# Kernel optimization log

Hardware: AMD Instinct MI355X
Metric: run time of the kernel (lower is better)

Reference implementation:

```python
import jax, jax.numpy as jnp
import numpy as np
from jax import lax

B, N, NIN, NOUT, K = 8, 4096, 64, 128, 32
RATIO, R = 0.25, 0.15
M = int(N * RATIO)
DIM = NIN + 4       # x_j concat 4 point-pair features


def setup_inputs() -> dict:
    key = jax.random.key(0)
    ks = jax.random.split(key, 10)
    x = jax.random.normal(ks[0], (B, N, NIN), jnp.float32)
    pos = jax.random.uniform(ks[1], (B, N, 3), jnp.float32)
    nrm = jax.random.normal(ks[2], (B, N, 3), jnp.float32)
    norm = nrm / jnp.linalg.norm(nrm, axis=-1, keepdims=True)
    batch = jnp.broadcast_to(jnp.arange(B, dtype=jnp.int32)[:, None], (B, N))
    s = 0.05
    W1 = jax.random.normal(ks[3], (DIM, DIM), jnp.float32) * s
    b1 = jnp.zeros((DIM,), jnp.float32)
    W2 = jax.random.normal(ks[4], (DIM, DIM), jnp.float32) * s
    b2 = jnp.zeros((DIM,), jnp.float32)
    W3 = jax.random.normal(ks[5], (DIM, NOUT), jnp.float32) * s
    b3 = jnp.zeros((NOUT,), jnp.float32)
    return dict(x=x, pos=pos, norm=norm, batch=batch,
                W1=W1, b1=b1, W2=W2, b2=b2, W3=W3, b3=b3)


def fps(pos):
    """Farthest point sampling, deterministic start at index 0. pos: [N,3] -> [M] int32."""
    n = pos.shape[0]
    def step(carry, _):
        dists, last = carry
        d = jnp.sum((pos - pos[last]) ** 2, axis=-1)
        dists = jnp.minimum(dists, d)
        nxt = jnp.argmax(dists).astype(jnp.int32)
        return (dists, nxt), last
    init = (jnp.full((n,), jnp.inf, pos.dtype), jnp.int32(0))
    (_, _), idx = lax.scan(step, init, None, length=M)
    return idx


def _angle(v1, v2):
    c = jnp.cross(v1, v2)
    return jnp.arctan2(jnp.linalg.norm(c, axis=-1), jnp.sum(v1 * v2, axis=-1))


def reference(x, pos, norm, batch, W1, b1, W2, b2, W3, b3):
    # batch is implicit in the leading B dim (equal-size clouds); arg kept for parity.
    idx = jax.vmap(fps)(pos)                                   # [B,M]
    pos_s = jnp.take_along_axis(pos, idx[..., None], axis=1)   # [B,M,3]
    norm_s = jnp.take_along_axis(norm, idx[..., None], axis=1) # [B,M,3]

    # radius neighbor search: K nearest within R per sampled center
    d2 = jnp.sum((pos_s[:, :, None, :] - pos[:, None, :, :]) ** 2, axis=-1)  # [B,M,N]
    masked = jnp.where(d2 <= R * R, d2, jnp.inf)
    negv, nbr = lax.top_k(-masked, K)                          # [B,M,K]
    valid = jnp.isfinite(negv)                                 # self always valid (d2=0)

    gather = jax.vmap(lambda a, i: a[i])                       # per-batch fancy gather
    x_j = gather(x, nbr)        # [B,M,K,NIN]
    pos_j = gather(pos, nbr)    # [B,M,K,3]
    norm_j = gather(norm, nbr)  # [B,M,K,3]

    d = pos_j - pos_s[:, :, None, :]                           # pos_j - pos_i
    n_i = jnp.broadcast_to(norm_s[:, :, None, :], norm_j.shape)
    ppf = jnp.stack([
        jnp.linalg.norm(d, axis=-1),
        _angle(n_i, d),
        _angle(norm_j, d),
        _angle(n_i, norm_j),
    ], axis=-1)                                                # [B,M,K,4]

    msg = jnp.concatenate([x_j, ppf], axis=-1)                 # [B,M,K,DIM]
    h = jax.nn.relu(msg @ W1 + b1)
    h = jax.nn.relu(h @ W2 + b2)
    h = jnp.where(valid[..., None], h, -jnp.inf)
    agg = jnp.max(h, axis=2)                                   # max aggregation [B,M,DIM]
    out = jax.nn.relu(agg @ W3 + b3)                           # global_nn [B,M,NOUT]
    return out, pos_s, idx
```

## Files before the change

### kernel.cpp

```cpp
#include <hip/hip_runtime.h>
#include <hip/hip_bf16.h>
#include <math.h>

#define BB 8
#define NN 4096
#define NIN 64
#define NOUTF 128
#define KNB 32
#define MM 1024
#define DIM 68
#define CAP 320

typedef float f32x2 __attribute__((ext_vector_type(2)));

template <int CTRL>
__device__ __forceinline__ float dppmax(float v)
{
    int m = __builtin_amdgcn_update_dpp(__float_as_int(v), __float_as_int(v),
                                        CTRL, 0xF, 0xF, false);
    return fmaxf(v, __int_as_float(m));
}

__global__ __launch_bounds__(256) void fps_kernel(
    const float* __restrict__ pos,
    int* __restrict__ idx_ws, float* __restrict__ pos_s_ws,
    float* __restrict__ out_pos_s, float* __restrict__ out_idx)
{
#pragma clang fp contract(off)
    __shared__ float4 redP[2][4];
    __shared__ int    redN[2][4];

    const int b    = blockIdx.x;
    const int tid  = threadIdx.x;
    const int wv   = tid >> 6;
    const int lane = tid & 63;
    const float* pb = pos + (size_t)b * NN * 3;

    f32x2 X[8], Y[8], Z[8], D[8];
#pragma unroll
    for (int j = 0; j < 8; ++j) {
        int pA = tid * 16 + 2 * j;
        X[j].x = pb[pA * 3 + 0]; X[j].y = pb[pA * 3 + 3];
        Y[j].x = pb[pA * 3 + 1]; Y[j].y = pb[pA * 3 + 4];
        Z[j].x = pb[pA * 3 + 2]; Z[j].y = pb[pA * 3 + 5];
        D[j].x = INFINITY;       D[j].y = INFINITY;
    }

    int   last = 0;
    float lx = pb[0], ly = pb[1], lz = pb[2];

    for (int t = 0; t < MM; ++t) {
        if (tid == 0) {
            idx_ws[b * MM + t]  = last;
            out_idx[b * MM + t] = (float)last;
            pos_s_ws[(b * MM + t) * 3 + 0] = lx;
            pos_s_ws[(b * MM + t) * 3 + 1] = ly;
            pos_s_ws[(b * MM + t) * 3 + 2] = lz;
            out_pos_s[(b * MM + t) * 3 + 0] = lx;
            out_pos_s[(b * MM + t) * 3 + 1] = ly;
            out_pos_s[(b * MM + t) * 3 + 2] = lz;
        }

        f32x2 lx2; lx2.x = lx; lx2.y = lx;
        f32x2 ly2; ly2.x = ly; ly2.y = ly;
        f32x2 lz2; lz2.x = lz; lz2.y = lz;

        float bv = -INFINITY;
        int   kloc = 0;
#pragma unroll
        for (int j = 0; j < 8; ++j) {
            f32x2 dx = X[j] - lx2;
            f32x2 dy = Y[j] - ly2;
            f32x2 dz = Z[j] - lz2;
            f32x2 s  = (dx * dx + dy * dy) + dz * dz;
            float n0 = fminf(D[j].x, s.x);
            float n1 = fminf(D[j].y, s.y);
            D[j].x = n0; D[j].y = n1;
            if (n0 > bv) { bv = n0; kloc = 2 * j; }
            if (n1 > bv) { bv = n1; kloc = 2 * j + 1; }
        }

        int jj = kloc >> 1;
        f32x2 xa = (jj & 1) ? X[1] : X[0];
        f32x2 xb = (jj & 1) ? X[3] : X[2];
        f32x2 xc = (jj & 1) ? X[5] : X[4];
        f32x2 xd = (jj & 1) ? X[7] : X[6];
        f32x2 xe = (jj & 2) ? xb : xa;
        f32x2 xf = (jj & 2) ? xd : xc;
        f32x2 xg = (jj & 4) ? xf : xe;
        float bx = (kloc & 1) ? xg.y : xg.x;

        f32x2 ya = (jj & 1) ? Y[1] : Y[0];
        f32x2 yb = (jj & 1) ? Y[3] : Y[2];
        f32x2 yc = (jj & 1) ? Y[5] : Y[4];
        f32x2 yd = (jj & 1) ? Y[7] : Y[6];
        f32x2 ye = (jj & 2) ? yb : ya;
        f32x2 yf = (jj & 2) ? yd : yc;
        f32x2 yg = (jj & 4) ? yf : ye;
        float by = (kloc & 1) ? yg.y : yg.x;

        f32x2 za = (jj & 1) ? Z[1] : Z[0];
        f32x2 zb = (jj & 1) ? Z[3] : Z[2];
        f32x2 zc = (jj & 1) ? Z[5] : Z[4];
        f32x2 zd = (jj & 1) ? Z[7] : Z[6];
        f32x2 ze = (jj & 2) ? zb : za;
        f32x2 zf = (jj & 2) ? zd : zc;
        f32x2 zg = (jj & 4) ? zf : ze;
        float bz = (kloc & 1) ? zg.y : zg.x;

        float r = bv;
        r = dppmax<0x111>(r);
        r = dppmax<0x112>(r);
        r = dppmax<0x114>(r);
        r = dppmax<0x118>(r);
        r = dppmax<0x142>(r);
        r = dppmax<0x143>(r);
        float wmax = __int_as_float(__builtin_amdgcn_readlane(__float_as_int(r), 63));

        unsigned long long msk = __ballot(bv == wmax);
        int wl = __ffsll(msk) - 1;

        const int p_ = t & 1;
        if (lane == wl) {
            redP[p_][wv] = make_float4(bx, by, bz, bv);
            redN[p_][wv] = tid * 16 + kloc;
        }
        __syncthreads();

        float4 e0 = redP[p_][0], e1 = redP[p_][1], e2 = redP[p_][2], e3 = redP[p_][3];
        int    i0 = redN[p_][0], i1 = redN[p_][1], i2 = redN[p_][2], i3 = redN[p_][3];

        float cv = e0.w; int ci = i0;
        float cx = e0.x, cy = e0.y, cz = e0.z;
        {
            bool bt = (e1.w > cv) || (e1.w == cv && i1 < ci);
            cv = bt ? e1.w : cv; ci = bt ? i1 : ci;
            cx = bt ? e1.x : cx; cy = bt ? e1.y : cy; cz = bt ? e1.z : cz;
        }
        {
            bool bt = (e2.w > cv) || (e2.w == cv && i2 < ci);
            cv = bt ? e2.w : cv; ci = bt ? i2 : ci;
            cx = bt ? e2.x : cx; cy = bt ? e2.y : cy; cz = bt ? e2.z : cz;
        }
        {
            bool bt = (e3.w > cv) || (e3.w == cv && i3 < ci);
            cv = bt ? e3.w : cv; ci = bt ? i3 : ci;
            cx = bt ? e3.x : cx; cy = bt ? e3.y : cy; cz = bt ? e3.z : cz;
        }
        last = ci; lx = cx; ly = cy; lz = cz;
    }
}

__global__ __launch_bounds__(256) void radius_kernel(
    const float* __restrict__ pos,
    const float* __restrict__ pos_s_ws,
    int* __restrict__ nbr_ws, int* __restrict__ nvalid_ws)
{
    __shared__ float d2L[4][CAP];
    __shared__ int   idL[4][CAP];
    __shared__ int   cntL[4];

    const int wv = threadIdx.x >> 6, lane = threadIdx.x & 63;
    const int c = blockIdx.x * 4 + wv;
    const int b = c >> 10;
    const float RSQ = 0.0225f;

    if (lane == 0) cntL[wv] = 0;

    float cx = pos_s_ws[c * 3 + 0];
    float cy = pos_s_ws[c * 3 + 1];
    float cz = pos_s_ws[c * 3 + 2];
    const float* pb = pos + (size_t)b * NN * 3;

    for (int it = 0; it < NN / 64; ++it) {
        int p = it * 64 + lane;
        float dx = __fsub_rn(cx, pb[p * 3 + 0]);
        float dy = __fsub_rn(cy, pb[p * 3 + 1]);
        float dz = __fsub_rn(cz, pb[p * 3 + 2]);
        float d2 = __fadd_rn(__fadd_rn(__fmul_rn(dx, dx), __fmul_rn(dy, dy)),
                             __fmul_rn(dz, dz));
        if (d2 <= RSQ) {
            int slot = atomicAdd(&cntL[wv], 1);
            if (slot < CAP) { d2L[wv][slot] = d2; idL[wv][slot] = p; }
        }
    }
    int n = cntL[wv];
    if (n > CAP) n = CAP;

    if (n <= KNB) {
        if (lane == 0) nvalid_ws[c] = n;
        if (lane < n) nbr_ws[c * KNB + lane] = idL[wv][lane];
    } else {
        if (lane == 0) nvalid_ws[c] = KNB;
        for (int a = lane; a < n; a += 64) {
            float da = d2L[wv][a]; int ia = idL[wv][a];
            int r = 0;
            for (int jj = 0; jj < n; ++jj) {
                float dj = d2L[wv][jj]; int ij = idL[wv][jj];
                r += (dj < da || (dj == da && ij < ia)) ? 1 : 0;
            }
            if (r < KNB) nbr_ws[c * KNB + r] = ia;
        }
    }
}

__device__ __forceinline__ float angle3(float ax, float ay, float az,
                                        float bx, float by, float bz)
{
    float cx = ay * bz - az * by;
    float cy = az * bx - ax * bz;
    float cz = ax * by - ay * bx;
    float cn = sqrtf(cx * cx + cy * cy + cz * cz);
    float dt = ax * bx + ay * by + az * bz;
    return atan2f(cn, dt);
}

__device__ __forceinline__ void layer_pass(const float* __restrict__ inL,
                                           const float* __restrict__ Ws,
                                           const float* __restrict__ bs,
                                           float* __restrict__ outL, int t)
{
    const int e = t & 63, wvi = t >> 6;
    for (int jg = wvi; jg < 17; jg += 4) {
        float ax = bs[jg * 4 + 0];
        float ay = bs[jg * 4 + 1];
        float az = bs[jg * 4 + 2];
        float aw = bs[jg * 4 + 3];
#pragma unroll 4
        for (int i = 0; i < DIM; ++i) {
            float m = inL[e * 69 + i];
            const float4 w = *reinterpret_cast<const float4*>(Ws + i * DIM + jg * 4);
            ax = fmaf(m, w.x, ax);
            ay = fmaf(m, w.y, ay);
            az = fmaf(m, w.z, az);
            aw = fmaf(m, w.w, aw);
        }
        outL[e * 69 + jg * 4 + 0] = fmaxf(ax, 0.0f);
        outL[e * 69 + jg * 4 + 1] = fmaxf(ay, 0.0f);
        outL[e * 69 + jg * 4 + 2] = fmaxf(az, 0.0f);
        outL[e * 69 + jg * 4 + 3] = fmaxf(aw, 0.0f);
    }
}

__global__ __launch_bounds__(256) void mlp_kernel(
    const float* __restrict__ x, const float* __restrict__ pos,
    const float* __restrict__ norm,
    const float* __restrict__ W1, const float* __restrict__ b1,
    const float* __restrict__ W2, const float* __restrict__ b2,
    const float* __restrict__ W3, const float* __restrict__ b3,
    const int* __restrict__ idx_ws, const float* __restrict__ pos_s_ws,
    const int* __restrict__ nbr_ws, const int* __restrict__ nvalid_ws,
    float* __restrict__ out)
{
    __shared__ alignas(16) float W1s[DIM * DIM];
    __shared__ alignas(16) float W2s[DIM * DIM];
    __shared__ float b1s[DIM], b2s[DIM];
    __shared__ float msgL[64 * 69];
    __shared__ float h1L[64 * 69];
    __shared__ float aggL[2 * DIM];
    __shared__ int   nvL[2], jLs[64];

    const int t = threadIdx.x;
    const int cg0 = blockIdx.x * 2;

    for (int u = t; u < DIM * DIM; u += 256) { W1s[u] = W1[u]; W2s[u] = W2[u]; }
    if (t < DIM) { b1s[t] = b1[t]; b2s[t] = b2[t]; }
    if (t < 2) nvL[t] = min(nvalid_ws[cg0 + t], KNB);
    __syncthreads();

    const int e = t & 63, fc = t >> 6;
    const int lc = e >> 5, slot = e & 31;
    const int c = cg0 + lc;
    const int b = c >> 10;

    if (fc == 0) {
        int nv = nvL[lc];
        jLs[e] = (slot < nv) ? nbr_ws[c * KNB + slot] : 0;
    }
    __syncthreads();

    const int j = jLs[e];
    {
        const float* xj = x + ((size_t)b * NN + j) * NIN + fc * 16;
#pragma unroll
        for (int r = 0; r < 4; ++r) {
            float4 v = *reinterpret_cast<const float4*>(xj + r * 4);
            msgL[e * 69 + fc * 16 + r * 4 + 0] = v.x;
            msgL[e * 69 + fc * 16 + r * 4 + 1] = v.y;
            msgL[e * 69 + fc * 16 + r * 4 + 2] = v.z;
            msgL[e * 69 + fc * 16 + r * 4 + 3] = v.w;
        }
    }
    if (fc == 0) {
        float pix = pos_s_ws[c * 3 + 0];
        float piy = pos_s_ws[c * 3 + 1];
        float piz = pos_s_ws[c * 3 + 2];
        int ic = idx_ws[c];
        const float* pj_ = pos  + ((size_t)b * NN + j) * 3;
        const float* nj_ = norm + ((size_t)b * NN + j) * 3;
        const float* ni_ = norm + ((size_t)b * NN + ic) * 3;
        float dx = pj_[0] - pix, dy = pj_[1] - piy, dz = pj_[2] - piz;
        float nix = ni_[0], niy = ni_[1], niz = ni_[2];
        float njx = nj_[0], njy = nj_[1], njz = nj_[2];
        msgL[e * 69 + 64] = sqrtf(dx * dx + dy * dy + dz * dz);
        msgL[e * 69 + 65] = angle3(nix, niy, niz, dx, dy, dz);
        msgL[e * 69 + 66] = angle3(njx, njy, njz, dx, dy, dz);
        msgL[e * 69 + 67] = angle3(nix, niy, niz, njx, njy, njz);
    }
    __syncthreads();

    layer_pass(msgL, W1s, b1s, h1L, t);
    __syncthreads();
    layer_pass(h1L, W2s, b2s, msgL, t);
    __syncthreads();

    if (t < 2 * DIM) {
        int cc = t / DIM, jf = t % DIM;
        int nv = nvL[cc];
        float v = -INFINITY;
        for (int s = 0; s < nv; ++s)
            v = fmaxf(v, msgL[(cc * 32 + s) * 69 + jf]);
        aggL[cc * DIM + jf] = v;
    }
    __syncthreads();

    {
        int cc = t >> 7, o = t & 127;
        int cgl = cg0 + cc;
        float acc = b3[o];
#pragma unroll 4
        for (int i = 0; i < DIM; ++i)
            acc = fmaf(aggL[cc * DIM + i], W3[i * NOUTF + o], acc);
        out[(size_t)cgl * NOUTF + o] = fmaxf(acc, 0.0f);
    }
}

extern "C" void kernel_launch(void* const* d_in, const int* in_sizes, int n_in,
                              void* d_out, int out_size, void* d_ws, size_t ws_size,
                              hipStream_t stream)
{
    const float* x    = (const float*)d_in[0];
    const float* pos  = (const float*)d_in[1];
    const float* norm = (const float*)d_in[2];
    const float* W1 = (const float*)d_in[4];
    const float* b1 = (const float*)d_in[5];
    const float* W2 = (const float*)d_in[6];
    const float* b2 = (const float*)d_in[7];
    const float* W3 = (const float*)d_in[8];
    const float* b3 = (const float*)d_in[9];

    float* out       = (float*)d_out;
    float* out_pos_s = out + (size_t)BB * MM * NOUTF;
    float* out_idx   = out_pos_s + (size_t)BB * MM * 3;

    char* ws = (char*)d_ws;
    int*   idx_ws    = (int*)ws;
    float* pos_s_ws  = (float*)(ws + 32768);
    int*   nbr_ws    = (int*)(ws + 131072);
    int*   nvalid_ws = (int*)(ws + 131072 + (size_t)BB * MM * KNB * 4);

    fps_kernel<<<dim3(BB), dim3(256), 0, stream>>>(pos, idx_ws, pos_s_ws,
                                                   out_pos_s, out_idx);
    radius_kernel<<<dim3((BB * MM) / 4), dim3(256), 0, stream>>>(pos, pos_s_ws,
                                                                 nbr_ws, nvalid_ws);
    mlp_kernel<<<dim3((BB * MM) / 2), dim3(256), 0, stream>>>(
        x, pos, norm, W1, b1, W2, b2, W3, b3,
        idx_ws, pos_s_ws, nbr_ws, nvalid_ws, out);
}
```

Before: 1.196 ms.

## Widen FPS block to 512 threads and defer argmax index recovery to winner lane

The FPS kernel now runs 512 threads with 8 points per thread instead of 256 with 16, halving the serial per-thread distance update per iteration. The per-thread argmax becomes a packed max tree, and the winning point's index and coordinates are recovered only in the winning lane by equality search after the wave reduction. The cross-wave reduction grows from 4 to 8 entries, and equality-based index recovery picks the lowest local index, which keeps tie behaviour consistent with first-occurrence argmax.

```diff
diff --git a/kernel.cpp b/kernel.cpp
--- a/kernel.cpp
+++ b/kernel.cpp
@@ -13,6 +13,15 @@
 
 typedef float f32x2 __attribute__((ext_vector_type(2)));
 
+__device__ __forceinline__ f32x2 pkmin(f32x2 a, f32x2 b)
+{
+    f32x2 r; r.x = fminf(a.x, b.x); r.y = fminf(a.y, b.y); return r;
+}
+__device__ __forceinline__ f32x2 pkmax(f32x2 a, f32x2 b)
+{
+    f32x2 r; r.x = fmaxf(a.x, b.x); r.y = fmaxf(a.y, b.y); return r;
+}
+
 template <int CTRL>
 __device__ __forceinline__ float dppmax(float v)
 {
@@ -21,14 +30,14 @@
     return fmaxf(v, __int_as_float(m));
 }
 
-__global__ __launch_bounds__(256) void fps_kernel(
+__global__ __launch_bounds__(512) void fps_kernel(
     const float* __restrict__ pos,
     int* __restrict__ idx_ws, float* __restrict__ pos_s_ws,
     float* __restrict__ out_pos_s, float* __restrict__ out_idx)
 {
 #pragma clang fp contract(off)
-    __shared__ float4 redP[2][4];
-    __shared__ int    redN[2][4];
+    __shared__ float4 redP[2][8];
+    __shared__ int    redN[2][8];
 
     const int b    = blockIdx.x;
     const int tid  = threadIdx.x;
@@ -36,10 +45,10 @@
     const int lane = tid & 63;
     const float* pb = pos + (size_t)b * NN * 3;
 
-    f32x2 X[8], Y[8], Z[8], D[8];
+    f32x2 X[4], Y[4], Z[4], D[4];
 #pragma unroll
-    for (int j = 0; j < 8; ++j) {
-        int pA = tid * 16 + 2 * j;
+    for (int j = 0; j < 4; ++j) {
+        int pA = tid * 8 + 2 * j;
         X[j].x = pb[pA * 3 + 0]; X[j].y = pb[pA * 3 + 3];
         Y[j].x = pb[pA * 3 + 1]; Y[j].y = pb[pA * 3 + 4];
         Z[j].x = pb[pA * 3 + 2]; Z[j].y = pb[pA * 3 + 5];
@@ -65,48 +74,18 @@
         f32x2 ly2; ly2.x = ly; ly2.y = ly;
         f32x2 lz2; lz2.x = lz; lz2.y = lz;
 
-        float bv = -INFINITY;
-        int   kloc = 0;
 #pragma unroll
-        for (int j = 0; j < 8; ++j) {
+        for (int j = 0; j < 4; ++j) {
             f32x2 dx = X[j] - lx2;
             f32x2 dy = Y[j] - ly2;
             f32x2 dz = Z[j] - lz2;
             f32x2 s  = (dx * dx + dy * dy) + dz * dz;
-            float n0 = fminf(D[j].x, s.x);
-            float n1 = fminf(D[j].y, s.y);
-            D[j].x = n0; D[j].y = n1;
-            if (n0 > bv) { bv = n0; kloc = 2 * j; }
-            if (n1 > bv) { bv = n1; kloc = 2 * j + 1; }
-        }
-
-        int jj = kloc >> 1;
-        f32x2 xa = (jj & 1) ? X[1] : X[0];
-        f32x2 xb = (jj & 1) ? X[3] : X[2];
-        f32x2 xc = (jj & 1) ? X[5] : X[4];
-        f32x2 xd = (jj & 1) ? X[7] : X[6];
-        f32x2 xe = (jj & 2) ? xb : xa;
-        f32x2 xf = (jj & 2) ? xd : xc;
-        f32x2 xg = (jj & 4) ? xf : xe;
-        float bx = (kloc & 1) ? xg.y : xg.x;
-
-        f32x2 ya = (jj & 1) ? Y[1] : Y[0];
-        f32x2 yb = (jj & 1) ? Y[3] : Y[2];
-        f32x2 yc = (jj & 1) ? Y[5] : Y[4];
-        f32x2 yd = (jj & 1) ? Y[7] : Y[6];
-        f32x2 ye = (jj & 2) ? yb : ya;
-        f32x2 yf = (jj & 2) ? yd : yc;
-        f32x2 yg = (jj & 4) ? yf : ye;
-        float by = (kloc & 1) ? yg.y : yg.x;
-
-        f32x2 za = (jj & 1) ? Z[1] : Z[0];
-        f32x2 zb = (jj & 1) ? Z[3] : Z[2];
-        f32x2 zc = (jj & 1) ? Z[5] : Z[4];
-        f32x2 zd = (jj & 1) ? Z[7] : Z[6];
-        f32x2 ze = (jj & 2) ? zb : za;
-        f32x2 zf = (jj & 2) ? zd : zc;
-        f32x2 zg = (jj & 4) ? zf : ze;
-        float bz = (kloc & 1) ? zg.y : zg.x;
+            D[j] = pkmin(D[j], s);
+        }
+        f32x2 m01 = pkmax(D[0], D[1]);
+        f32x2 m23 = pkmax(D[2], D[3]);
+        f32x2 mm  = pkmax(m01, m23);
+        float bv  = fmaxf(mm.x, mm.y);
 
         float r = bv;
         r = dppmax<0x111>(r);
@@ -122,30 +101,46 @@
 
         const int p_ = t & 1;
         if (lane == wl) {
+            int k = 7;
+            if (D[3].y == bv) k = 7;
+            if (D[3].x == bv) k = 6;
+            if (D[2].y == bv) k = 5;
+            if (D[2].x == bv) k = 4;
+            if (D[1].y == bv) k = 3;
+            if (D[1].x == bv) k = 2;
+            if (D[0].y == bv) k = 1;
+            if (D[0].x == bv) k = 0;
+            int jj = k >> 1;
+
+            f32x2 xa = (jj & 1) ? X[1] : X[0];
+            f32x2 xb = (jj & 1) ? X[3] : X[2];
+            f32x2 xe = (jj & 2) ? xb : xa;
+            float bx = (k & 1) ? xe.y : xe.x;
+
+            f32x2 ya = (jj & 1) ? Y[1] : Y[0];
+            f32x2 yb = (jj & 1) ? Y[3] : Y[2];
+            f32x2 ye = (jj & 2) ? yb : ya;
+            float by = (k & 1) ? ye.y : ye.x;
+
+            f32x2 za = (jj & 1) ? Z[1] : Z[0];
+            f32x2 zb = (jj & 1) ? Z[3] : Z[2];
+            f32x2 ze = (jj & 2) ? zb : za;
+            float bz = (k & 1) ? ze.y : ze.x;
+
             redP[p_][wv] = make_float4(bx, by, bz, bv);
-            redN[p_][wv] = tid * 16 + kloc;
+            redN[p_][wv] = tid * 8 + k;
         }
         __syncthreads();
 
-        float4 e0 = redP[p_][0], e1 = redP[p_][1], e2 = redP[p_][2], e3 = redP[p_][3];
-        int    i0 = redN[p_][0], i1 = redN[p_][1], i2 = redN[p_][2], i3 = redN[p_][3];
-
-        float cv = e0.w; int ci = i0;
+        float4 e0 = redP[p_][0];
+        float cv = e0.w; int ci = redN[p_][0];
         float cx = e0.x, cy = e0.y, cz = e0.z;
-        {
-            bool bt = (e1.w > cv) || (e1.w == cv && i1 < ci);
-            cv = bt ? e1.w : cv; ci = bt ? i1 : ci;
-            cx = bt ? e1.x : cx; cy = bt ? e1.y : cy; cz = bt ? e1.z : cz;
-        }
-        {
-            bool bt = (e2.w > cv) || (e2.w == cv && i2 < ci);
-            cv = bt ? e2.w : cv; ci = bt ? i2 : ci;
-            cx = bt ? e2.x : cx; cy = bt ? e2.y : cy; cz = bt ? e2.z : cz;
-        }
-        {
-            bool bt = (e3.w > cv) || (e3.w == cv && i3 < ci);
-            cv = bt ? e3.w : cv; ci = bt ? i3 : ci;
-            cx = bt ? e3.x : cx; cy = bt ? e3.y : cy; cz = bt ? e3.z : cz;
+#pragma unroll
+        for (int w = 1; w < 8; ++w) {
+            float4 ew = redP[p_][w]; int iw = redN[p_][w];
+            bool bt = (ew.w > cv) || (ew.w == cv && iw < ci);
+            cv = bt ? ew.w : cv; ci = bt ? iw : ci;
+            cx = bt ? ew.x : cx; cy = bt ? ew.y : cy; cz = bt ? ew.z : cz;
         }
         last = ci; lx = cx; ly = cy; lz = cz;
     }
@@ -359,7 +354,7 @@
     int*   nbr_ws    = (int*)(ws + 131072);
     int*   nvalid_ws = (int*)(ws + 131072 + (size_t)BB * MM * KNB * 4);
 
-    fps_kernel<<<dim3(BB), dim3(256), 0, stream>>>(pos, idx_ws, pos_s_ws,
+    fps_kernel<<<dim3(BB), dim3(512), 0, stream>>>(pos, idx_ws, pos_s_ws,
                                                    out_pos_s, out_idx);
     radius_kernel<<<dim3((BB * MM) / 4), dim3(256), 0, stream>>>(pos, pos_s_ws,
                                                                  nbr_ws, nvalid_ws);
```

Result: slower. 1.487 ms (+24.4%).

## Restructure FPS argmax: tree max, index-only reduction, LDS position lookup

Applied to the files above, without the earlier changes.

The per-thread sequential compare-and-track argmax is replaced by a packed max tree followed by a first-match index search. The winning coordinates are no longer selected through register mux trees; instead the whole cloud is staged into 64KB of LDS as float4 and the winner's position is read back by index after the cross-wave reduction. The aim is to shorten the serial dependency chain in each of the 1024 FPS iterations. In exchange it adds an extra LDS read on the critical path and heavy LDS use per block.

```diff
diff --git a/kernel.cpp b/kernel.cpp
--- a/kernel.cpp
+++ b/kernel.cpp
@@ -13,6 +13,11 @@
 
 typedef float f32x2 __attribute__((ext_vector_type(2)));
 
+__device__ __forceinline__ f32x2 pkmax(f32x2 a, f32x2 b)
+{
+    f32x2 r; r.x = fmaxf(a.x, b.x); r.y = fmaxf(a.y, b.y); return r;
+}
+
 template <int CTRL>
 __device__ __forceinline__ float dppmax(float v)
 {
@@ -27,8 +32,8 @@
     float* __restrict__ out_pos_s, float* __restrict__ out_idx)
 {
 #pragma clang fp contract(off)
-    __shared__ float4 redP[2][4];
-    __shared__ int    redN[2][4];
+    __shared__ float4 posL[NN];
+    __shared__ f32x2  slot[2][4];
 
     const int b    = blockIdx.x;
     const int tid  = threadIdx.x;
@@ -45,6 +50,13 @@
         Z[j].x = pb[pA * 3 + 2]; Z[j].y = pb[pA * 3 + 5];
         D[j].x = INFINITY;       D[j].y = INFINITY;
     }
+#pragma unroll
+    for (int j = 0; j < 16; ++j) {
+        int p2 = tid + 256 * j;
+        posL[p2] = make_float4(pb[p2 * 3 + 0], pb[p2 * 3 + 1],
+                               pb[p2 * 3 + 2], 0.0f);
+    }
+    __syncthreads();
 
     int   last = 0;
     float lx = pb[0], ly = pb[1], lz = pb[2];
@@ -65,48 +77,32 @@
         f32x2 ly2; ly2.x = ly; ly2.y = ly;
         f32x2 lz2; lz2.x = lz; lz2.y = lz;
 
-        float bv = -INFINITY;
-        int   kloc = 0;
 #pragma unroll
         for (int j = 0; j < 8; ++j) {
             f32x2 dx = X[j] - lx2;
             f32x2 dy = Y[j] - ly2;
             f32x2 dz = Z[j] - lz2;
             f32x2 s  = (dx * dx + dy * dy) + dz * dz;
-            float n0 = fminf(D[j].x, s.x);
-            float n1 = fminf(D[j].y, s.y);
-            D[j].x = n0; D[j].y = n1;
-            if (n0 > bv) { bv = n0; kloc = 2 * j; }
-            if (n1 > bv) { bv = n1; kloc = 2 * j + 1; }
-        }
-
-        int jj = kloc >> 1;
-        f32x2 xa = (jj & 1) ? X[1] : X[0];
-        f32x2 xb = (jj & 1) ? X[3] : X[2];
-        f32x2 xc = (jj & 1) ? X[5] : X[4];
-        f32x2 xd = (jj & 1) ? X[7] : X[6];
-        f32x2 xe = (jj & 2) ? xb : xa;
-        f32x2 xf = (jj & 2) ? xd : xc;
-        f32x2 xg = (jj & 4) ? xf : xe;
-        float bx = (kloc & 1) ? xg.y : xg.x;
-
-        f32x2 ya = (jj & 1) ? Y[1] : Y[0];
-        f32x2 yb = (jj & 1) ? Y[3] : Y[2];
-        f32x2 yc = (jj & 1) ? Y[5] : Y[4];
-        f32x2 yd = (jj & 1) ? Y[7] : Y[6];
-        f32x2 ye = (jj & 2) ? yb : ya;
-        f32x2 yf = (jj & 2) ? yd : yc;
-        f32x2 yg = (jj & 4) ? yf : ye;
-        float by = (kloc & 1) ? yg.y : yg.x;
-
-        f32x2 za = (jj & 1) ? Z[1] : Z[0];
-        f32x2 zb = (jj & 1) ? Z[3] : Z[2];
-        f32x2 zc = (jj & 1) ? Z[5] : Z[4];
-        f32x2 zd = (jj & 1) ? Z[7] : Z[6];
-        f32x2 ze = (jj & 2) ? zb : za;
-        f32x2 zf = (jj & 2) ? zd : zc;
-        f32x2 zg = (jj & 4) ? zf : ze;
-        float bz = (kloc & 1) ? zg.y : zg.x;
+            D[j].x = fminf(D[j].x, s.x);
+            D[j].y = fminf(D[j].y, s.y);
+        }
+        f32x2 m0 = pkmax(pkmax(D[0], D[1]), pkmax(D[2], D[3]));
+        f32x2 m1 = pkmax(pkmax(D[4], D[5]), pkmax(D[6], D[7]));
+        f32x2 mm = pkmax(m0, m1);
+        float bv = fmaxf(mm.x, mm.y);
+
+        int k0 = (D[0].x == bv) ? 0  : ((D[0].y == bv) ? 1  : 16);
+        int k1 = (D[1].x == bv) ? 2  : ((D[1].y == bv) ? 3  : 16);
+        int k2 = (D[2].x == bv) ? 4  : ((D[2].y == bv) ? 5  : 16);
+        int k3 = (D[3].x == bv) ? 6  : ((D[3].y == bv) ? 7  : 16);
+        int k4 = (D[4].x == bv) ? 8  : ((D[4].y == bv) ? 9  : 16);
+        int k5 = (D[5].x == bv) ? 10 : ((D[5].y == bv) ? 11 : 16);
+        int k6 = (D[6].x == bv) ? 12 : ((D[6].y == bv) ? 13 : 16);
+        int k7 = (D[7].x == bv) ? 14 : ((D[7].y == bv) ? 15 : 16);
+        k0 = min(k0, k4); k1 = min(k1, k5); k2 = min(k2, k6); k3 = min(k3, k7);
+        k0 = min(k0, k2); k1 = min(k1, k3);
+        int kmin = min(k0, k1);
+        int p_cand = tid * 16 + kmin;
 
         float r = bv;
         r = dppmax<0x111>(r);
@@ -118,36 +114,37 @@
         float wmax = __int_as_float(__builtin_amdgcn_readlane(__float_as_int(r), 63));
 
         unsigned long long msk = __ballot(bv == wmax);
-        int wl = __ffsll(msk) - 1;
+        int wl = __ffsll((long long)msk) - 1;
+        int pwin_wave = __builtin_amdgcn_readlane(p_cand, wl);
 
         const int p_ = t & 1;
-        if (lane == wl) {
-            redP[p_][wv] = make_float4(bx, by, bz, bv);
-            redN[p_][wv] = tid * 16 + kloc;
+        if (lane == 0) {
+            f32x2 sv; sv.x = wmax; sv.y = __int_as_float(pwin_wave);
+            slot[p_][wv] = sv;
         }
         __syncthreads();
 
-        float4 e0 = redP[p_][0], e1 = redP[p_][1], e2 = redP[p_][2], e3 = redP[p_][3];
-        int    i0 = redN[p_][0], i1 = redN[p_][1], i2 = redN[p_][2], i3 = redN[p_][3];
-
-        float cv = e0.w; int ci = i0;
-        float cx = e0.x, cy = e0.y, cz = e0.z;
+        f32x2 s0 = slot[p_][0], s1 = slot[p_][1];
+        f32x2 s2 = slot[p_][2], s3 = slot[p_][3];
+        float cv = s0.x; int ci = __float_as_int(s0.y);
         {
-            bool bt = (e1.w > cv) || (e1.w == cv && i1 < ci);
-            cv = bt ? e1.w : cv; ci = bt ? i1 : ci;
-            cx = bt ? e1.x : cx; cy = bt ? e1.y : cy; cz = bt ? e1.z : cz;
+            int i1 = __float_as_int(s1.y);
+            bool bt = (s1.x > cv) || (s1.x == cv && i1 < ci);
+            cv = bt ? s1.x : cv; ci = bt ? i1 : ci;
         }
         {
-            bool bt = (e2.w > cv) || (e2.w == cv && i2 < ci);
-            cv = bt ? e2.w : cv; ci = bt ? i2 : ci;
-            cx = bt ? e2.x : cx; cy = bt ? e2.y : cy; cz = bt ? e2.z : cz;
+            int i2 = __float_as_int(s2.y);
+            bool bt = (s2.x > cv) || (s2.x == cv && i2 < ci);
+            cv = bt ? s2.x : cv; ci = bt ? i2 : ci;
         }
         {
-            bool bt = (e3.w > cv) || (e3.w == cv && i3 < ci);
-            cv = bt ? e3.w : cv; ci = bt ? i3 : ci;
-            cx = bt ? e3.x : cx; cy = bt ? e3.y : cy; cz = bt ? e3.z : cz;
-        }
-        last = ci; lx = cx; ly = cy; lz = cz;
+            int i3 = __float_as_int(s3.y);
+            bool bt = (s3.x > cv) || (s3.x == cv && i3 < ci);
+            cv = bt ? s3.x : cv; ci = bt ? i3 : ci;
+        }
+
+        float4 cw = posL[ci];
+        last = ci; lx = cw.x; ly = cw.y; lz = cw.z;
     }
 }
 
```

New measurement: 1.065 ms. 1.12x faster.
